# Kernel optimization log

Hardware: AMD Instinct MI355X
Metric: run time of the kernel (lower is better)

The kernel has to match this reference:

```python
import jax, jax.numpy as jnp
import numpy as np

DT = 16.67
TAU1 = 100.0
TAU2 = 100.0
ALPHA_FF = 0.5
ALPHA_FB = 0.5
A1 = DT / TAU1
A2 = DT / TAU2


def setup_inputs() -> dict:
    key = jax.random.key(0)
    ks = jax.random.split(key, 8)
    B, T, I, H1, H2 = 64, 1024, 128, 256, 256
    def xavier(k, shape):
        fan_in, fan_out = shape[1], shape[0]
        lim = jnp.sqrt(6.0 / (fan_in + fan_out))
        return jax.random.uniform(k, shape, jnp.float32, -lim, lim)
    return {
        "x": jax.random.normal(ks[0], (B, T, I), jnp.float32),
        "seq_lengths": jax.random.randint(ks[1], (B,), 1, T + 1),
        "Wi": xavier(ks[2], (H1, I)),
        "bi": jnp.zeros((H1,), jnp.float32),
        "W11": xavier(ks[3], (H1, H1)),
        "W22": xavier(ks[4], (H2, H2)),
        "W12": xavier(ks[5], (H2, H1)),
        "W21": xavier(ks[6], (H1, H2)),
    }


def reference(x, seq_lengths, Wi, bi, W11, W22, W12, W21):
    B, T, _ = x.shape
    H1 = W11.shape[0]
    H2 = W22.shape[0]
    # mask[t, b] = 1.0 if t < seq_lengths[b]
    mask = (jnp.arange(T)[:, None] < seq_lengths[None, :]).astype(x.dtype)  # [T,B]
    # Precompute input projection for all steps (same math as per-step Linear)
    xproj = jnp.einsum('btI,hI->tbh', x, Wi) + bi  # [T,B,H1]

    def step(carry, inp):
        h1, h2 = carry
        xp, m = inp  # [B,H1], [B]
        pre1 = xp + h1 @ W11.T + (h2 @ W21.T) * ALPHA_FB
        h1n = jax.nn.relu(h1 * (1.0 - A1) + pre1 * A1)
        pre2 = h2 @ W22.T + (h1 @ W12.T) * ALPHA_FF  # uses old h1
        h2n = jax.nn.relu(h2 * (1.0 - A2) + pre2 * A2)
        m2 = m[:, None]
        # value-preserving; only cuts gradients when masked (as in torch detach trick)
        h1n = h1n * m2 + jax.lax.stop_gradient(h1n) * (1.0 - m2)
        h2n = h2n * m2 + jax.lax.stop_gradient(h2n) * (1.0 - m2)
        return (h1n, h2n), (h1n, h2n)

    h1_0 = jnp.zeros((B, H1), x.dtype)
    h2_0 = jnp.zeros((B, H2), x.dtype)
    (h1, h2), (o1, o2) = jax.lax.scan(step, (h1_0, h2_0), (xproj, mask))
    outputs = jnp.concatenate([o1, o2], axis=2)  # [T,B,H1+H2]
    outputs = jnp.swapaxes(outputs, 0, 1)        # [B,T,H1+H2]
    return outputs, h1, h2
```

## Files before the change

### kernel.cpp

```cpp
#include <hip/hip_runtime.h>

typedef short short8 __attribute__((ext_vector_type(8)));
typedef float f32x4 __attribute__((ext_vector_type(4)));
typedef unsigned int u32x4 __attribute__((ext_vector_type(4)));
typedef unsigned long long ull;

#define NB 64
#define NT 1024
#define NI 128
#define NH 512

#define WS_X     655360
#define WS_FLAGS 786432
#define WS_XCC   790528
#define WS_XP    1048576

#define SWZ(m) ((unsigned)(((m) & 7) << 3))

__device__ __forceinline__ unsigned short f2bf(float f) {
  union { float f; unsigned u; } v; v.f = f;
  unsigned u = v.u;
  return (unsigned short)((u + 0x7FFFu + ((u >> 16) & 1u)) >> 16);
}

__global__ __launch_bounds__(256) void buildM_k(
    const float* __restrict__ W11, const float* __restrict__ W22,
    const float* __restrict__ W12, const float* __restrict__ W21,
    unsigned short* __restrict__ M, unsigned* __restrict__ ctrl) {
  if (blockIdx.x == 0) {
    #pragma unroll
    for (int i = 0; i < 8; i++) ctrl[threadIdx.x + 256 * i] = 0;
  }
  int idx = blockIdx.x * 256 + threadIdx.x;
  int o = idx >> 9, k = idx & 511;
  const float A1f = (float)(16.67 / 100.0);
  float v;
  if (o < 256) {
    v = (k < 256) ? A1f * W11[(o << 8) + k]
                  : A1f * 0.5f * W21[(o << 8) + (k - 256)];
  } else {
    int o2 = o - 256;
    v = (k < 256) ? A1f * 0.5f * W12[(o2 << 8) + k]
                  : A1f * W22[(o2 << 8) + (k - 256)];
  }
  M[idx] = f2bf(v);
}

__global__ __launch_bounds__(256) void buildWiT_k(const float* __restrict__ Wi,
                                                  float* __restrict__ WiT) {
  int idx = blockIdx.x * 256 + threadIdx.x;
  int k = idx >> 8, o = idx & 255;
  WiT[idx] = Wi[o * 128 + k];
}

__global__ __launch_bounds__(256) void xproj_k(
    const float* __restrict__ x, const float* __restrict__ WiT,
    const float* __restrict__ bi, float* __restrict__ xp) {
  __shared__ float xs[128 * 68];
  int tid = threadIdx.x;
  int wv = tid >> 6;
  int c = tid & 63;
  long Rbase = (long)blockIdx.x * 64;
  const float* xg = x + Rbase * 128;
  #pragma unroll
  for (int i = 0; i < 32; i++) {
    int idx = tid + 256 * i;
    int r = idx >> 7, k = idx & 127;
    xs[k * 68 + r] = xg[idx];
  }
  __syncthreads();
  float acc[4][16];
  #pragma unroll
  for (int a = 0; a < 4; a++)
    #pragma unroll
    for (int b = 0; b < 16; b++) acc[a][b] = 0.f;
  for (int k = 0; k < 128; k++) {
    f32x4 w4 = *(const f32x4*)(WiT + k * 256 + 4 * c);
    const float* xr = &xs[k * 68 + 16 * wv];
    #pragma unroll
    for (int rr = 0; rr < 4; rr++) {
      f32x4 xv = *(const f32x4*)(xr + 4 * rr);
      #pragma unroll
      for (int cc = 0; cc < 4; cc++) {
        #pragma unroll
        for (int u = 0; u < 4; u++)
          acc[cc][4 * rr + u] = fmaf(w4[cc], xv[u], acc[cc][4 * rr + u]);
      }
    }
  }
  f32x4 bv = *(const f32x4*)(bi + 4 * c);
  const float A1f = (float)(16.67 / 100.0);
  #pragma unroll
  for (int rr = 0; rr < 16; rr++) {
    long R = Rbase + 16 * wv + rr;
    int b = (int)(R >> 10), t = (int)(R & 1023);
    f32x4 o;
    #pragma unroll
    for (int cc = 0; cc < 4; cc++) o[cc] = A1f * (acc[cc][rr] + bv[cc]);
    *(f32x4*)(xp + ((long)(t * 64 + b) << 8) + 4 * c) = o;
  }
}

#define PINQ(W, R0, R1, R2, R3)                                   \
  asm volatile("v_accvgpr_write_b32 " R0 ", %0\n\t"               \
               "v_accvgpr_write_b32 " R1 ", %1\n\t"               \
               "v_accvgpr_write_b32 " R2 ", %2\n\t"               \
               "v_accvgpr_write_b32 " R3 ", %3"                   \
               :: "v"((W)[0]), "v"((W)[1]), "v"((W)[2]), "v"((W)[3]) \
               : R0, R1, R2, R3)

#define MF "v_mfma_f32_16x16x32_bf16 "
#define KTG_B(AV, S0, S1, PRE, POST)                                  \
  asm volatile(PRE MF "%0, %1, " S0 ", %0" : "+v"(acc[0]) : "v"(AV)); \
  asm volatile(MF "%0, %1, " S1 ", %0" POST : "+v"(acc[1]) : "v"(AV));
#define KTG(i, S0, S1)  KTG_B(av[i], S0, S1, "", "")
#define KTGF(i, S0, S1) KTG_B(av[i], S0, S1, "s_nop 1\n\t", "")
#define KTGL(i, S0, S1) KTG_B(av[i], S0, S1, "", "\n\ts_nop 7\n\ts_nop 1")

__global__ __launch_bounds__(512, 2) void rnn_k(
    const unsigned short* __restrict__ M, const float* __restrict__ xp,
    float* __restrict__ out, char* __restrict__ ws) {
  const int bid = blockIdx.x;
  if (bid & 4) return;
  const int g = bid & 3;
  const int role = bid >> 3;
  const int prole = 1 - role;
  const int tid = threadIdx.x;
  const int w = tid >> 6;
  const int lane = tid & 63;
  const int n = lane & 15;
  const int q = lane >> 4;
  const int colbase = role * 256 + w * 32;
  const int pcolbase = prole * 256 + w * 32;

  __shared__ __align__(16) unsigned short hb[2][16 * 512];
  __shared__ int sFast;

  {
    uint4 z = {0, 0, 0, 0};
    uint4* p = (uint4*)&hb[0][0];
    p[tid] = z;
    p[tid + 512] = z;
  }

  unsigned* flags = (unsigned*)(ws + WS_FLAGS);
  unsigned* xcct = (unsigned*)(ws + WS_XCC);
  if (tid == 0) {
    unsigned myx;
    asm volatile("s_getreg_b32 %0, hwreg(HW_REG_XCC_ID)" : "=s"(myx));
    __hip_atomic_store(&xcct[bid], myx + 1, __ATOMIC_RELAXED, __HIP_MEMORY_SCOPE_AGENT);
    unsigned ox;
    while ((ox = __hip_atomic_load(&xcct[bid ^ 8], __ATOMIC_RELAXED,
                                   __HIP_MEMORY_SCOPE_AGENT)) == 0u)
      __builtin_amdgcn_s_sleep(2);
    sFast = (ox == myx + 1) ? 1 : 0;
  }

  const float C1 = (float)(1.0 - 16.67 / 100.0);

  {
    const unsigned short* mb0 = M + (colbase + 0 * 16 + n) * 512 + q * 8;
    const unsigned short* mb1 = M + (colbase + 1 * 16 + n) * 512 + q * 8;
#define WQ0(kt) (*(const u32x4*)(mb0 + (kt) * 32))
#define WQ1(kt) (*(const u32x4*)(mb1 + (kt) * 32))
    PINQ(WQ0(0),  "a0",   "a1",   "a2",   "a3");
    PINQ(WQ1(0),  "a4",   "a5",   "a6",   "a7");
    PINQ(WQ0(1),  "a8",   "a9",   "a10",  "a11");
    PINQ(WQ1(1),  "a12",  "a13",  "a14",  "a15");
    PINQ(WQ0(2),  "a16",  "a17",  "a18",  "a19");
    PINQ(WQ1(2),  "a20",  "a21",  "a22",  "a23");
    PINQ(WQ0(3),  "a24",  "a25",  "a26",  "a27");
    PINQ(WQ1(3),  "a28",  "a29",  "a30",  "a31");
    PINQ(WQ0(4),  "a32",  "a33",  "a34",  "a35");
    PINQ(WQ1(4),  "a36",  "a37",  "a38",  "a39");
    PINQ(WQ0(5),  "a40",  "a41",  "a42",  "a43");
    PINQ(WQ1(5),  "a44",  "a45",  "a46",  "a47");
    PINQ(WQ0(6),  "a48",  "a49",  "a50",  "a51");
    PINQ(WQ1(6),  "a52",  "a53",  "a54",  "a55");
    PINQ(WQ0(7),  "a56",  "a57",  "a58",  "a59");
    PINQ(WQ1(7),  "a60",  "a61",  "a62",  "a63");
    PINQ(WQ0(8),  "a64",  "a65",  "a66",  "a67");
    PINQ(WQ1(8),  "a68",  "a69",  "a70",  "a71");
    PINQ(WQ0(9),  "a72",  "a73",  "a74",  "a75");
    PINQ(WQ1(9),  "a76",  "a77",  "a78",  "a79");
    PINQ(WQ0(10), "a80",  "a81",  "a82",  "a83");
    PINQ(WQ1(10), "a84",  "a85",  "a86",  "a87");
    PINQ(WQ0(11), "a88",  "a89",  "a90",  "a91");
    PINQ(WQ1(11), "a92",  "a93",  "a94",  "a95");
    PINQ(WQ0(12), "a96",  "a97",  "a98",  "a99");
    PINQ(WQ1(12), "a100", "a101", "a102", "a103");
    PINQ(WQ0(13), "a104", "a105", "a106", "a107");
    PINQ(WQ1(13), "a108", "a109", "a110", "a111");
    PINQ(WQ0(14), "a112", "a113", "a114", "a115");
    PINQ(WQ1(14), "a116", "a117", "a118", "a119");
    PINQ(WQ0(15), "a120", "a121", "a122", "a123");
    PINQ(WQ1(15), "a124", "a125", "a126", "a127");
  }

  float hprev[2][4];
  #pragma unroll
  for (int a = 0; a < 2; a++)
    #pragma unroll
    for (int b = 0; b < 4; b++) hprev[a][b] = 0.f;

  const bool hasxp = (role == 0);
  const float* xpb = xp + ((g * 16 + 4 * q) << 8) + colbase + n;
  float xpA[2][4], xpB[2][4];
  #pragma unroll
  for (int a = 0; a < 2; a++)
    #pragma unroll
    for (int b = 0; b < 4; b++) { xpA[a][b] = 0.f; xpB[a][b] = 0.f; }
  if (hasxp) {
    #pragma unroll
    for (int nt = 0; nt < 2; nt++)
      #pragma unroll
      for (int j = 0; j < 4; j++) {
        xpA[nt][j] = __builtin_nontemporal_load(xpb + 0L * 16384 + j * 256 + nt * 16);
        xpB[nt][j] = __builtin_nontemporal_load(xpb + 1L * 16384 + j * 256 + nt * 16);
      }
  }

  float* outb = out + (long)(g * 16 + 4 * q) * (NT * NH) + colbase + n;

  char* Xb = ws + WS_X;
  char* xs0 = Xb + ((g * 2 + role) * 2 + 0) * 8192 + tid * 16;
  char* xs1 = Xb + ((g * 2 + role) * 2 + 1) * 8192 + tid * 16;
  const char* xr0 = Xb + ((g * 2 + prole) * 2 + 0) * 8192 + tid * 16;
  const char* xr1 = Xb + ((g * 2 + prole) * 2 + 1) * 8192 + tid * 16;
  unsigned* fs = flags + ((g * 2 + role) * 8 + w) * 16;
  unsigned* fr = flags + ((g * 2 + prole) * 8 + w) * 16;

  __syncthreads();
  const bool fastp = (sFast != 0);

  auto step = [&](unsigned short* hr, unsigned short* hw, int t,
                  float (&xpc)[2][4]) {
    const int role8 = role * 8, prole8 = prole * 8;
    short8 av[8];

    #pragma unroll
    for (int i = 0; i < 8; i++) {
      int kt = role8 + i;
      av[i] = *(const short8*)(hr + ((unsigned)(n * 512 + kt * 32 + q * 8) ^ SWZ(n)));
    }
    asm volatile("" ::: "memory");

    unsigned pd[4];
    if (t > 0) {
      const char* xb = (t & 1) ? xr1 : xr0;
      if (fastp) {
        while (*(volatile const unsigned*)fr < (unsigned)t)
          __builtin_amdgcn_s_sleep(1);
        volatile const unsigned* xv = (volatile const unsigned*)xb;
        #pragma unroll
        for (int i = 0; i < 4; i++) pd[i] = xv[i];
      } else {
        while (__hip_atomic_load(fr, __ATOMIC_RELAXED,
                                 __HIP_MEMORY_SCOPE_AGENT) < (unsigned)t)
          __builtin_amdgcn_s_sleep(1);
        #pragma unroll
        for (int i = 0; i < 2; i++) {
          ull u = __hip_atomic_load((const ull*)(xb + 8 * i), __ATOMIC_RELAXED,
                                    __HIP_MEMORY_SCOPE_AGENT);
          pd[2 * i] = (unsigned)u;
          pd[2 * i + 1] = (unsigned)(u >> 32);
        }
      }
    }

    f32x4 acc[2];
    acc[0] = (f32x4){0.f, 0.f, 0.f, 0.f};
    acc[1] = (f32x4){0.f, 0.f, 0.f, 0.f};

    if (role == 0) {
      KTGF(0, "a[0:3]",    "a[4:7]");
      KTG (1, "a[8:11]",   "a[12:15]");
      KTG (2, "a[16:19]",  "a[20:23]");
      KTG (3, "a[24:27]",  "a[28:31]");
      KTG (4, "a[32:35]",  "a[36:39]");
      KTG (5, "a[40:43]",  "a[44:47]");
      KTG (6, "a[48:51]",  "a[52:55]");
      KTG (7, "a[56:59]",  "a[60:63]");
    } else {
      KTGF(0, "a[64:67]",  "a[68:71]");
      KTG (1, "a[72:75]",  "a[76:79]");
      KTG (2, "a[80:83]",  "a[84:87]");
      KTG (3, "a[88:91]",  "a[92:95]");
      KTG (4, "a[96:99]",  "a[100:103]");
      KTG (5, "a[104:107]","a[108:111]");
      KTG (6, "a[112:115]","a[116:119]");
      KTG (7, "a[120:123]","a[124:127]");
    }

    if (t > 0) {
      #pragma unroll
      for (int nt = 0; nt < 2; nt++) {
        #pragma unroll
        for (int jh = 0; jh < 2; jh++) {
          unsigned dv = pd[nt * 2 + jh];
          int r0 = 4 * q + 2 * jh, r1 = r0 + 1;
          int c = pcolbase + nt * 16 + n;
          hr[(unsigned)(r0 * 512 + c) ^ SWZ(r0)] = (unsigned short)dv;
          hr[(unsigned)(r1 * 512 + c) ^ SWZ(r1)] = (unsigned short)(dv >> 16);
        }
      }
    }
    asm volatile("s_waitcnt lgkmcnt(0)\n\ts_barrier" ::: "memory");

    #pragma unroll
    for (int i = 0; i < 8; i++) {
      int kt = prole8 + i;
      av[i] = *(const short8*)(hr + ((unsigned)(n * 512 + kt * 32 + q * 8) ^ SWZ(n)));
    }
    asm volatile("" ::: "memory");

    if (role == 0) {
      KTG (0, "a[64:67]",  "a[68:71]");
      KTG (1, "a[72:75]",  "a[76:79]");
      KTG (2, "a[80:83]",  "a[84:87]");
      KTG (3, "a[88:91]",  "a[92:95]");
      KTG (4, "a[96:99]",  "a[100:103]");
      KTG (5, "a[104:107]","a[108:111]");
      KTG (6, "a[112:115]","a[116:119]");
      KTGL(7, "a[120:123]","a[124:127]");
    } else {
      KTG (0, "a[0:3]",    "a[4:7]");
      KTG (1, "a[8:11]",   "a[12:15]");
      KTG (2, "a[16:19]",  "a[20:23]");
      KTG (3, "a[24:27]",  "a[28:31]");
      KTG (4, "a[32:35]",  "a[36:39]");
      KTG (5, "a[40:43]",  "a[44:47]");
      KTG (6, "a[48:51]",  "a[52:55]");
      KTGL(7, "a[56:59]",  "a[60:63]");
    }

    unsigned dw[4];
    #pragma unroll
    for (int nt = 0; nt < 2; nt++) {
      #pragma unroll
      for (int j = 0; j < 4; j++) {
        float v = fmaf(hprev[nt][j], C1, acc[nt][j] + xpc[nt][j]);
        v = fmaxf(v, 0.f);
        hprev[nt][j] = v;
      }
      asm("v_cvt_pk_bf16_f32 %0, %1, %2"
          : "=v"(dw[nt * 2]) : "v"(hprev[nt][0]), "v"(hprev[nt][1]));
      asm("v_cvt_pk_bf16_f32 %0, %1, %2"
          : "=v"(dw[nt * 2 + 1]) : "v"(hprev[nt][2]), "v"(hprev[nt][3]));
    }
    {
      char* xb = ((t + 1) & 1) ? xs1 : xs0;
      if (fastp) {
        uint4 v0 = {dw[0], dw[1], dw[2], dw[3]};
        *(uint4*)xb = v0;
        asm volatile("s_waitcnt vmcnt(0)" ::: "memory");
        if (lane == 0) *(volatile unsigned*)fs = (unsigned)(t + 1);
      } else {
        #pragma unroll
        for (int i = 0; i < 2; i++) {
          ull u = (ull)dw[2 * i] | ((ull)dw[2 * i + 1] << 32);
          __hip_atomic_store((ull*)(xb + 8 * i), u, __ATOMIC_RELAXED,
                             __HIP_MEMORY_SCOPE_AGENT);
        }
        if (lane == 0)
          __hip_atomic_store(fs, (unsigned)(t + 1), __ATOMIC_RELEASE,
                             __HIP_MEMORY_SCOPE_AGENT);
      }
    }
    if (hasxp) {
      int tn = t + 2; if (tn >= NT) tn = 0;
      const float* xpl = xpb + (long)tn * 16384;
      #pragma unroll
      for (int nt = 0; nt < 2; nt++)
        #pragma unroll
        for (int j = 0; j < 4; j++)
          xpc[nt][j] = __builtin_nontemporal_load(xpl + j * 256 + nt * 16);
    }
    #pragma unroll
    for (int nt = 0; nt < 2; nt++) {
      #pragma unroll
      for (int jh = 0; jh < 2; jh++) {
        unsigned dv = dw[nt * 2 + jh];
        int r0 = 4 * q + 2 * jh, r1 = r0 + 1;
        int c = colbase + nt * 16 + n;
        hw[(unsigned)(r0 * 512 + c) ^ SWZ(r0)] = (unsigned short)dv;
        hw[(unsigned)(r1 * 512 + c) ^ SWZ(r1)] = (unsigned short)(dv >> 16);
      }
    }
    float* outt = outb + (long)t * NH;
    #pragma unroll
    for (int nt = 0; nt < 2; nt++)
      #pragma unroll
      for (int j = 0; j < 4; j++)
        __builtin_nontemporal_store(hprev[nt][j],
                                    outt + (long)j * (NT * NH) + nt * 16);
    asm volatile("s_waitcnt lgkmcnt(0)\n\ts_barrier" ::: "memory");
  };

  #pragma unroll 1
  for (int t = 0; t < NT; t += 2) {
    step(hb[0], hb[1], t, xpA);
    step(hb[1], hb[0], t + 1, xpB);
  }

  const long fbase = (long)NB * NT * NH;
  #pragma unroll
  for (int nt = 0; nt < 2; nt++) {
    #pragma unroll
    for (int j = 0; j < 4; j++) {
      int b = g * 16 + 4 * q + j;
      int col = colbase + nt * 16 + n;
      long off = (col < 256) ? (fbase + b * 256 + col)
                             : (fbase + 16384 + b * 256 + (col - 256));
      out[off] = hprev[nt][j];
    }
  }
}

extern "C" void kernel_launch(void* const* d_in, const int* in_sizes, int n_in,
                              void* d_out, int out_size, void* d_ws, size_t ws_size,
                              hipStream_t stream) {
  const float* x   = (const float*)d_in[0];
  const float* Wi  = (const float*)d_in[2];
  const float* bi  = (const float*)d_in[3];
  const float* W11 = (const float*)d_in[4];
  const float* W22 = (const float*)d_in[5];
  const float* W12 = (const float*)d_in[6];
  const float* W21 = (const float*)d_in[7];
  float* out = (float*)d_out;

  unsigned short* M = (unsigned short*)d_ws;
  float* WiT = (float*)((char*)d_ws + 524288);
  unsigned* ctrl = (unsigned*)((char*)d_ws + WS_FLAGS);
  float* xp = (float*)((char*)d_ws + WS_XP);

  buildM_k<<<1024, 256, 0, stream>>>(W11, W22, W12, W21, M, ctrl);
  buildWiT_k<<<128, 256, 0, stream>>>(Wi, WiT);
  xproj_k<<<1024, 256, 0, stream>>>(x, WiT, bi, xp);
  rnn_k<<<16, 512, 0, stream>>>(M, xp, out, (char*)d_ws);
}
```

Baseline: 2.730 ms.

## Move peer hidden-state exchange to end of step, removing mid-step barrier

```diff
diff --git a/kernel.cpp b/kernel.cpp
--- a/kernel.cpp
+++ b/kernel.cpp
@@ -235,104 +235,33 @@
 
   auto step = [&](unsigned short* hr, unsigned short* hw, int t,
                   float (&xpc)[2][4]) {
-    const int role8 = role * 8, prole8 = prole * 8;
     short8 av[8];
-
-    #pragma unroll
-    for (int i = 0; i < 8; i++) {
-      int kt = role8 + i;
-      av[i] = *(const short8*)(hr + ((unsigned)(n * 512 + kt * 32 + q * 8) ^ SWZ(n)));
-    }
-    asm volatile("" ::: "memory");
-
-    unsigned pd[4];
-    if (t > 0) {
-      const char* xb = (t & 1) ? xr1 : xr0;
-      if (fastp) {
-        while (*(volatile const unsigned*)fr < (unsigned)t)
-          __builtin_amdgcn_s_sleep(1);
-        volatile const unsigned* xv = (volatile const unsigned*)xb;
-        #pragma unroll
-        for (int i = 0; i < 4; i++) pd[i] = xv[i];
-      } else {
-        while (__hip_atomic_load(fr, __ATOMIC_RELAXED,
-                                 __HIP_MEMORY_SCOPE_AGENT) < (unsigned)t)
-          __builtin_amdgcn_s_sleep(1);
-        #pragma unroll
-        for (int i = 0; i < 2; i++) {
-          ull u = __hip_atomic_load((const ull*)(xb + 8 * i), __ATOMIC_RELAXED,
-                                    __HIP_MEMORY_SCOPE_AGENT);
-          pd[2 * i] = (unsigned)u;
-          pd[2 * i + 1] = (unsigned)(u >> 32);
-        }
-      }
-    }
-
     f32x4 acc[2];
     acc[0] = (f32x4){0.f, 0.f, 0.f, 0.f};
     acc[1] = (f32x4){0.f, 0.f, 0.f, 0.f};
 
-    if (role == 0) {
-      KTGF(0, "a[0:3]",    "a[4:7]");
-      KTG (1, "a[8:11]",   "a[12:15]");
-      KTG (2, "a[16:19]",  "a[20:23]");
-      KTG (3, "a[24:27]",  "a[28:31]");
-      KTG (4, "a[32:35]",  "a[36:39]");
-      KTG (5, "a[40:43]",  "a[44:47]");
-      KTG (6, "a[48:51]",  "a[52:55]");
-      KTG (7, "a[56:59]",  "a[60:63]");
-    } else {
-      KTGF(0, "a[64:67]",  "a[68:71]");
-      KTG (1, "a[72:75]",  "a[76:79]");
-      KTG (2, "a[80:83]",  "a[84:87]");
-      KTG (3, "a[88:91]",  "a[92:95]");
-      KTG (4, "a[96:99]",  "a[100:103]");
-      KTG (5, "a[104:107]","a[108:111]");
-      KTG (6, "a[112:115]","a[116:119]");
-      KTG (7, "a[120:123]","a[124:127]");
-    }
-
-    if (t > 0) {
-      #pragma unroll
-      for (int nt = 0; nt < 2; nt++) {
-        #pragma unroll
-        for (int jh = 0; jh < 2; jh++) {
-          unsigned dv = pd[nt * 2 + jh];
-          int r0 = 4 * q + 2 * jh, r1 = r0 + 1;
-          int c = pcolbase + nt * 16 + n;
-          hr[(unsigned)(r0 * 512 + c) ^ SWZ(r0)] = (unsigned short)dv;
-          hr[(unsigned)(r1 * 512 + c) ^ SWZ(r1)] = (unsigned short)(dv >> 16);
-        }
-      }
-    }
-    asm volatile("s_waitcnt lgkmcnt(0)\n\ts_barrier" ::: "memory");
-
-    #pragma unroll
-    for (int i = 0; i < 8; i++) {
-      int kt = prole8 + i;
-      av[i] = *(const short8*)(hr + ((unsigned)(n * 512 + kt * 32 + q * 8) ^ SWZ(n)));
-    }
-    asm volatile("" ::: "memory");
-
-    if (role == 0) {
-      KTG (0, "a[64:67]",  "a[68:71]");
-      KTG (1, "a[72:75]",  "a[76:79]");
-      KTG (2, "a[80:83]",  "a[84:87]");
-      KTG (3, "a[88:91]",  "a[92:95]");
-      KTG (4, "a[96:99]",  "a[100:103]");
-      KTG (5, "a[104:107]","a[108:111]");
-      KTG (6, "a[112:115]","a[116:119]");
-      KTGL(7, "a[120:123]","a[124:127]");
-    } else {
-      KTG (0, "a[0:3]",    "a[4:7]");
-      KTG (1, "a[8:11]",   "a[12:15]");
-      KTG (2, "a[16:19]",  "a[20:23]");
-      KTG (3, "a[24:27]",  "a[28:31]");
-      KTG (4, "a[32:35]",  "a[36:39]");
-      KTG (5, "a[40:43]",  "a[44:47]");
-      KTG (6, "a[48:51]",  "a[52:55]");
-      KTGL(7, "a[56:59]",  "a[60:63]");
-    }
+    #pragma unroll
+    for (int i = 0; i < 8; i++)
+      av[i] = *(const short8*)(hr + ((unsigned)(n * 512 + i * 32 + q * 8) ^ SWZ(n)));
+    KTGF(0, "a[0:3]",    "a[4:7]");
+    KTG (1, "a[8:11]",   "a[12:15]");
+    KTG (2, "a[16:19]",  "a[20:23]");
+    KTG (3, "a[24:27]",  "a[28:31]");
+    KTG (4, "a[32:35]",  "a[36:39]");
+    KTG (5, "a[40:43]",  "a[44:47]");
+    KTG (6, "a[48:51]",  "a[52:55]");
+    KTG (7, "a[56:59]",  "a[60:63]");
+    #pragma unroll
+    for (int i = 0; i < 8; i++)
+      av[i] = *(const short8*)(hr + ((unsigned)(n * 512 + (8 + i) * 32 + q * 8) ^ SWZ(n)));
+    KTG (0, "a[64:67]",  "a[68:71]");
+    KTG (1, "a[72:75]",  "a[76:79]");
+    KTG (2, "a[80:83]",  "a[84:87]");
+    KTG (3, "a[88:91]",  "a[92:95]");
+    KTG (4, "a[96:99]",  "a[100:103]");
+    KTG (5, "a[104:107]","a[108:111]");
+    KTG (6, "a[112:115]","a[116:119]");
+    KTGL(7, "a[120:123]","a[124:127]");
 
     unsigned dw[4];
     #pragma unroll
@@ -348,6 +277,7 @@
       asm("v_cvt_pk_bf16_f32 %0, %1, %2"
           : "=v"(dw[nt * 2 + 1]) : "v"(hprev[nt][2]), "v"(hprev[nt][3]));
     }
+
     {
       char* xb = ((t + 1) & 1) ? xs1 : xs0;
       if (fastp) {
@@ -367,15 +297,7 @@
                              __HIP_MEMORY_SCOPE_AGENT);
       }
     }
-    if (hasxp) {
-      int tn = t + 2; if (tn >= NT) tn = 0;
-      const float* xpl = xpb + (long)tn * 16384;
-      #pragma unroll
-      for (int nt = 0; nt < 2; nt++)
-        #pragma unroll
-        for (int j = 0; j < 4; j++)
-          xpc[nt][j] = __builtin_nontemporal_load(xpl + j * 256 + nt * 16);
-    }
+
     #pragma unroll
     for (int nt = 0; nt < 2; nt++) {
       #pragma unroll
@@ -394,6 +316,49 @@
       for (int j = 0; j < 4; j++)
         __builtin_nontemporal_store(hprev[nt][j],
                                     outt + (long)j * (NT * NH) + nt * 16);
+    if (hasxp) {
+      int tn = t + 2; if (tn >= NT) tn = 0;
+      const float* xpl = xpb + (long)tn * 16384;
+      #pragma unroll
+      for (int nt = 0; nt < 2; nt++)
+        #pragma unroll
+        for (int j = 0; j < 4; j++)
+          xpc[nt][j] = __builtin_nontemporal_load(xpl + j * 256 + nt * 16);
+    }
+
+    {
+      unsigned pd[4];
+      const char* xb = ((t + 1) & 1) ? xr1 : xr0;
+      if (fastp) {
+        while (*(volatile const unsigned*)fr < (unsigned)(t + 1))
+          __builtin_amdgcn_s_sleep(1);
+        volatile const unsigned* xv = (volatile const unsigned*)xb;
+        #pragma unroll
+        for (int i = 0; i < 4; i++) pd[i] = xv[i];
+      } else {
+        while (__hip_atomic_load(fr, __ATOMIC_RELAXED,
+                                 __HIP_MEMORY_SCOPE_AGENT) < (unsigned)(t + 1))
+          __builtin_amdgcn_s_sleep(1);
+        #pragma unroll
+        for (int i = 0; i < 2; i++) {
+          ull u = __hip_atomic_load((const ull*)(xb + 8 * i), __ATOMIC_RELAXED,
+                                    __HIP_MEMORY_SCOPE_AGENT);
+          pd[2 * i] = (unsigned)u;
+          pd[2 * i + 1] = (unsigned)(u >> 32);
+        }
+      }
+      #pragma unroll
+      for (int nt = 0; nt < 2; nt++) {
+        #pragma unroll
+        for (int jh = 0; jh < 2; jh++) {
+          unsigned dv = pd[nt * 2 + jh];
+          int r0 = 4 * q + 2 * jh, r1 = r0 + 1;
+          int c = pcolbase + nt * 16 + n;
+          hw[(unsigned)(r0 * 512 + c) ^ SWZ(r0)] = (unsigned short)dv;
+          hw[(unsigned)(r1 * 512 + c) ^ SWZ(r1)] = (unsigned short)(dv >> 16);
+        }
+      }
+    }
     asm volatile("s_waitcnt lgkmcnt(0)\n\ts_barrier" ::: "memory");
   };
 
```

Result: faster. 2.595 ms (-4.9%).
